# Optimization experiments

Hardware: AMD Instinct MI355X
Metric: run time of the kernel (lower is better)

Reference implementation:

```python
import jax, jax.numpy as jnp
import numpy as np

B, T, C, H = 4, 1024, 1024, 16
D = C // H
SINK = 4
EPS_LN = 1e-5

def _layernorm(x, w, b):
    mu = jnp.mean(x, axis=-1, keepdims=True)
    var = jnp.mean(jnp.square(x - mu), axis=-1, keepdims=True)
    return (x - mu) * jax.lax.rsqrt(var + EPS_LN) * w + b

def setup_inputs() -> dict:
    key = jax.random.key(0)
    ks = jax.random.split(key, 8)
    s = 0.02
    inp = {
        "x": jax.random.normal(ks[0], (B, T, C), jnp.float32),
        "attention_mask": jnp.ones((B, T), jnp.int32),
        "W_attn": jax.random.normal(ks[1], (C, 3 * C), jnp.float32) * s,
        "b_attn": jnp.zeros((3 * C,), jnp.float32),
        "W_proj": jax.random.normal(ks[2], (C, C), jnp.float32) * s,
        "b_proj": jnp.zeros((C,), jnp.float32),
        "ln1_w": jnp.ones((C,), jnp.float32),
        "ln1_b": jnp.zeros((C,), jnp.float32),
        "ln2_w": jnp.ones((C,), jnp.float32),
        "ln2_b": jnp.zeros((C,), jnp.float32),
        "W_fc": jax.random.normal(ks[3], (C, 4 * C), jnp.float32) * s,
        "b_fc": jnp.zeros((4 * C,), jnp.float32),
        "W_fc2": jax.random.normal(ks[4], (4 * C, C), jnp.float32) * s,
        "b_fc2": jnp.zeros((C,), jnp.float32),
        "threshold": jnp.float32((0 + 1) / 12 * 0.01),  # layer_idx=0, n_layer=12, final_token_threshold=0.01
    }
    return inp

def reference(x, attention_mask, W_attn, b_attn, W_proj, b_proj,
              ln1_w, ln1_b, ln2_w, ln2_b, W_fc, b_fc, W_fc2, b_fc2, threshold):
    # --- attention on ln_1(x), with explicit weight materialization ---
    h = _layernorm(x, ln1_w, ln1_b)
    qkv = h @ W_attn + b_attn                       # (B,T,3C)
    q, k, v = jnp.split(qkv, 3, axis=-1)
    q = q.reshape(B, T, H, D).transpose(0, 2, 1, 3)  # (B,H,T,D)
    k = k.reshape(B, T, H, D).transpose(0, 2, 1, 3)
    v = v.reshape(B, T, H, D).transpose(0, 2, 1, 3)
    scores = jnp.einsum("bhqd,bhkd->bhqk", q, k) * (1.0 / np.sqrt(D))
    causal = jnp.tril(jnp.ones((T, T), bool))[None, None]          # (1,1,T,T)
    keep = causal & (attention_mask[:, None, None, :] != 0)        # (B,1,T,T)
    scores = jnp.where(keep, scores, -jnp.inf)
    att = jax.nn.softmax(scores, axis=-1)
    att = jnp.nan_to_num(att, nan=0.0)              # fully-masked rows -> 0
    y = jnp.einsum("bhqk,bhkd->bhqd", att, v)       # (B,H,T,D)
    y = y.transpose(0, 2, 1, 3).reshape(B, T, C)
    y = y @ W_proj + b_proj                         # dropout=0.0 -> identity

    # --- cumulative-attention importance ---
    imp = att.sum(axis=2).mean(axis=1)              # (B,T): attention received
    pos_norm = jnp.arange(T, 0, -1, dtype=jnp.float32) / T
    imp = imp / (pos_norm[None, :] + 1e-8)
    imp = imp.at[:, :SINK].set(imp.max() + 1.0)

    # --- residual + MLP ---
    x2 = x + y
    m = _layernorm(x2, ln2_w, ln2_b)
    mlp = jax.nn.gelu(m @ W_fc + b_fc, approximate=False) @ W_fc2 + b_fc2
    out = x2 + mlp

    # --- hard pruning mask ---
    mask = (imp >= threshold).astype(jnp.float32)
    mask = mask.at[:, :SINK].set(1.0)
    mask = mask * attention_mask.astype(jnp.float32)
    return out, mask, imp
```

## Files before the change

### kernel.cpp

```cpp
#include <hip/hip_runtime.h>
#include <math.h>

constexpr int Bc = 4, Tc = 1024, Cc = 1024, Hc = 16, Dc = 64, SINKc = 4;
constexpr float EPS_LN = 1e-5f;

typedef __bf16 bf16x4 __attribute__((ext_vector_type(4)));
typedef __bf16 bf16x8 __attribute__((ext_vector_type(8)));
typedef float  f32x4  __attribute__((ext_vector_type(4)));

__global__ __launch_bounds__(256) void transpose_bf16(
    const float* __restrict__ W, __bf16* __restrict__ Wt, int K, int N)
{
    __shared__ float S[32][33];
    int n0 = blockIdx.x * 32, k0 = blockIdx.y * 32;
    int t = threadIdx.x;
    int r = t >> 3, c4 = (t & 7) * 4;
    float4 v = *(const float4*)(W + (size_t)(k0 + r) * N + n0 + c4);
    S[r][c4+0] = v.x; S[r][c4+1] = v.y; S[r][c4+2] = v.z; S[r][c4+3] = v.w;
    __syncthreads();
    bf16x4 o = { (__bf16)S[c4+0][r], (__bf16)S[c4+1][r],
                 (__bf16)S[c4+2][r], (__bf16)S[c4+3][r] };
    *(bf16x4*)(Wt + (size_t)(n0 + r) * K + k0 + c4) = o;
}

__global__ __launch_bounds__(256) void ln_kernel(
    const float* __restrict__ x, const float* __restrict__ w,
    const float* __restrict__ bsh, __bf16* __restrict__ outp)
{
    int row = blockIdx.x;
    const float* xr = x + (size_t)row * Cc;
    int tid = threadIdx.x;

    float4 xl = reinterpret_cast<const float4*>(xr)[tid];
    float s  = xl.x + xl.y + xl.z + xl.w;
    float s2 = xl.x*xl.x + xl.y*xl.y + xl.z*xl.z + xl.w*xl.w;
    for (int off = 32; off; off >>= 1) {
        s  += __shfl_down(s,  off, 64);
        s2 += __shfl_down(s2, off, 64);
    }
    __shared__ float r1[4], r2[4];
    if ((tid & 63) == 0) { r1[tid >> 6] = s; r2[tid >> 6] = s2; }
    __syncthreads();
    float mu  = (r1[0]+r1[1]+r1[2]+r1[3]) * (1.0f / Cc);
    float var = (r2[0]+r2[1]+r2[2]+r2[3]) * (1.0f / Cc) - mu*mu;
    float rstd = rsqrtf(var + EPS_LN);

    float4 wl = reinterpret_cast<const float4*>(w)[tid];
    float4 bl = reinterpret_cast<const float4*>(bsh)[tid];
    bf16x4 o = { (__bf16)((xl.x - mu) * rstd * wl.x + bl.x),
                 (__bf16)((xl.y - mu) * rstd * wl.y + bl.y),
                 (__bf16)((xl.z - mu) * rstd * wl.z + bl.z),
                 (__bf16)((xl.w - mu) * rstd * wl.w + bl.w) };
    *(bf16x4*)(outp + (size_t)row * Cc + tid * 4) = o;
}

template <int EPI, typename OutT, int TM, int OCC>
__global__ __launch_bounds__(256, OCC) void gemm_bf16(
    const __bf16* __restrict__ A, const __bf16* __restrict__ Bt,
    const float* __restrict__ bias, const float* R,
    OutT* Cm, int M, int N, int K)
{
    __shared__ __bf16 As[2][2][TM * 32];
    __shared__ __bf16 Bs[2][2][128 * 32];

    const int tid  = threadIdx.x;
    const int wave = tid >> 6, lane = tid & 63;
    const int wm = wave >> 1, wn = wave & 1;
    const int lr = lane & 15, lc = lane >> 4;

    const int gx = N >> 7;
    const int nblk = gridDim.x;
    const int per = nblk >> 3;
    const int rank = (blockIdx.x & 7) * per + (blockIdx.x >> 3);
    const int GM = 8;
    const int grp = rank / (GM * gx);
    const int rem = rank % (GM * gx);
    const int by = grp * GM + (rem % GM);
    const int bx = rem / GM;

    f32x4 acc[TM / 32][4] = {};

    const int srow = lane >> 2;
    const int cphys = lane & 3;

    auto stage = [&](int buf, int kk) {
        #pragma unroll
        for (int ii = wave; ii < (TM / 16) * 2; ii += 4) {
            int idx = ii >> 1, c = ii & 1;
            int rloc = idx * 16 + srow;
            int clog = (cphys - (rloc >> 1)) & 3;
            const __bf16* ga = A + (size_t)(by * TM + rloc) * K + kk + c * 32 + clog * 8;
            __builtin_amdgcn_global_load_lds(
                (const __attribute__((address_space(1))) void*)ga,
                (__attribute__((address_space(3))) void*)(&As[buf][c][idx * 512]), 16, 0, 0);
        }
        #pragma unroll
        for (int ii = wave; ii < 16; ii += 4) {
            int idx = ii >> 1, c = ii & 1;
            int rloc = idx * 16 + srow;
            int clog = (cphys - (rloc >> 1)) & 3;
            const __bf16* gb = Bt + (size_t)(bx * 128 + rloc) * K + kk + c * 32 + clog * 8;
            __builtin_amdgcn_global_load_lds(
                (const __attribute__((address_space(1))) void*)gb,
                (__attribute__((address_space(3))) void*)(&Bs[buf][c][idx * 512]), 16, 0, 0);
        }
    };

    stage(0, 0);
    __syncthreads();

    int cur = 0;
    for (int k0 = 0; k0 < K; k0 += 64) {
        if (k0 + 64 < K) stage(cur ^ 1, k0 + 64);

        #pragma unroll
        for (int s = 0; s < 2; s++) {
            bf16x8 af[TM / 32], bfr[4];
            #pragma unroll
            for (int i = 0; i < TM / 32; i++) {
                int ra = wm * (TM / 2) + i * 16 + lr;
                int ca = (lc + (ra >> 1)) & 3;
                af[i] = *(const bf16x8*)(&As[cur][s][ra * 32 + ca * 8]);
            }
            #pragma unroll
            for (int j = 0; j < 4; j++) {
                int rb = wn * 64 + j * 16 + lr;
                int cb = (lc + (rb >> 1)) & 3;
                bfr[j] = *(const bf16x8*)(&Bs[cur][s][rb * 32 + cb * 8]);
            }
            #pragma unroll
            for (int i = 0; i < TM / 32; i++)
                #pragma unroll
                for (int j = 0; j < 4; j++)
                    acc[i][j] = __builtin_amdgcn_mfma_f32_16x16x32_bf16(
                        af[i], bfr[j], acc[i][j], 0, 0, 0);
        }

        __syncthreads();
        cur ^= 1;
    }

    #pragma unroll
    for (int j = 0; j < 4; j++) {
        int n = bx * 128 + wn * 64 + j * 16 + lr;
        float bv = bias[n];
        #pragma unroll
        for (int i = 0; i < TM / 32; i++) {
            int m0 = by * TM + wm * (TM / 2) + i * 16 + lc * 4;
            #pragma unroll
            for (int e = 0; e < 4; e++) {
                float t = acc[i][j][e] + bv;
                if (EPI == 1) t = 0.5f * t * (1.0f + erff(t * 0.70710678118654752f));
                if (EPI == 2) t += R[(size_t)(m0 + e) * N + n];
                Cm[(size_t)(m0 + e) * N + n] = (OutT)t;
            }
        }
    }
}

__global__ __launch_bounds__(256, 3) void attn_mfma(
    const __bf16* __restrict__ qkv, const int* __restrict__ amask,
    __bf16* __restrict__ ybuf, float* __restrict__ lbuf)
{
    __shared__ __bf16 Kb[2][64 * 32];
    __shared__ __align__(16) __bf16 Vt[64][72];
    __shared__ __align__(16) __bf16 Ps[64][72];

    int blk = blockIdx.x;
    int idx = blk & 15, h = (blk >> 4) & 15, b = blk >> 8;
    int idx2 = (idx + h + b) & 15;
    int p2 = idx2 >> 1;
    int qt = (idx2 & 1) ? p2 : (15 - p2);
    int q0 = qt * 64;

    int tid = threadIdx.x, wave = tid >> 6, lane = tid & 63;
    int quad = lane >> 4, l15 = lane & 15;
    const int srow = lane >> 2, cphys = lane & 3;
    const size_t RS = 3 * Cc;
    const size_t bT = (size_t)b * Tc;

    bf16x8 qf[2];
    {
        const __bf16* qrow = qkv + (bT + q0 + wave * 16 + l15) * RS + h * 64 + quad * 8;
        qf[0] = *(const bf16x8*)qrow;
        qf[1] = *(const bf16x8*)(qrow + 32);
    }

    float l_part[4] = {0.f, 0.f, 0.f, 0.f};
    f32x4 Oacc[4] = {};

    for (int kt = 0; kt <= qt; kt++) {
        int k0 = kt * 64;
        __syncthreads();

        #pragma unroll
        for (int c = 0; c < 2; c++) {
            int rloc = wave * 16 + srow;
            int clog = (cphys - (rloc >> 1)) & 3;
            const __bf16* g = qkv + (bT + k0 + rloc) * RS + Cc + h * 64 + c * 32 + clog * 8;
            __builtin_amdgcn_global_load_lds(
                (const __attribute__((address_space(1))) void*)g,
                (__attribute__((address_space(3))) void*)(&Kb[c][wave * 512]), 16, 0, 0);
        }
        {
            int kk = lane, dbase = wave * 16;
            const __bf16* vrow = qkv + (bT + k0 + kk) * RS + 2 * Cc + h * 64 + dbase;
            bf16x8 v0 = *(const bf16x8*)vrow;
            bf16x8 v1 = *(const bf16x8*)(vrow + 8);
            #pragma unroll
            for (int j = 0; j < 8; j++) Vt[dbase + j][kk] = v0[j];
            #pragma unroll
            for (int j = 0; j < 8; j++) Vt[dbase + 8 + j][kk] = v1[j];
        }
        int am4[4];
        #pragma unroll
        for (int j = 0; j < 4; j++) am4[j] = amask[bT + k0 + j * 16 + l15];
        __syncthreads();

        f32x4 Sacc[4] = {};
        #pragma unroll
        for (int c = 0; c < 2; c++)
            #pragma unroll
            for (int j = 0; j < 4; j++) {
                int rb = j * 16 + l15;
                int cb = (quad + (rb >> 1)) & 3;
                bf16x8 kf = *(const bf16x8*)(&Kb[c][rb * 32 + cb * 8]);
                Sacc[j] = __builtin_amdgcn_mfma_f32_16x16x32_bf16(qf[c], kf, Sacc[j], 0, 0, 0);
            }

        #pragma unroll
        for (int e = 0; e < 4; e++) {
            int qg = q0 + wave * 16 + quad * 4 + e;
            #pragma unroll
            for (int j = 0; j < 4; j++) {
                int kg = k0 + j * 16 + l15;
                float p = (kg <= qg && am4[j] != 0)
                              ? __expf(Sacc[j][e] * 0.125f) : 0.f;
                l_part[e] += p;
                Ps[wave * 16 + quad * 4 + e][j * 16 + l15] = (__bf16)p;
            }
        }
        __syncthreads();

        #pragma unroll
        for (int c2 = 0; c2 < 2; c2++) {
            bf16x8 pa = *(const bf16x8*)(&Ps[wave * 16 + l15][quad * 8 + c2 * 32]);
            #pragma unroll
            for (int j2 = 0; j2 < 4; j2++) {
                bf16x8 vb = *(const bf16x8*)(&Vt[j2 * 16 + l15][quad * 8 + c2 * 32]);
                Oacc[j2] = __builtin_amdgcn_mfma_f32_16x16x32_bf16(pa, vb, Oacc[j2], 0, 0, 0);
            }
        }
    }

    #pragma unroll
    for (int e = 0; e < 4; e++) {
        float l = l_part[e];
        #pragma unroll
        for (int off = 8; off; off >>= 1) l += __shfl_xor(l, off, 64);
        int qg = q0 + wave * 16 + quad * 4 + e;
        float invl = (l > 0.f) ? 1.f / l : 0.f;
        #pragma unroll
        for (int j2 = 0; j2 < 4; j2++)
            ybuf[(bT + qg) * Cc + h * 64 + j2 * 16 + l15] = (__bf16)(Oacc[j2][e] * invl);
        if (l15 == 0)
            lbuf[(size_t)(b * Hc + h) * Tc + qg] = l;
    }
}

__global__ __launch_bounds__(256, 4) void imp_mfma(
    const __bf16* __restrict__ qkv, const int* __restrict__ amask,
    const float* __restrict__ lbuf, float* __restrict__ impbuf)
{
    __shared__ __bf16 Qb[2][64 * 32];
    __shared__ float rls[64];

    int blk = blockIdx.x;
    int idx = blk & 15, h = (blk >> 4) & 15, b = blk >> 8;
    int idx2 = (idx + h + b) & 15;
    int p2 = idx2 >> 1;
    int kt = (idx2 & 1) ? (15 - p2) : p2;
    int k0 = kt * 64;

    int tid = threadIdx.x, wave = tid >> 6, lane = tid & 63;
    int quad = lane >> 4, l15 = lane & 15;
    const int srow = lane >> 2, cphys = lane & 3;
    const size_t RS = 3 * Cc;
    const size_t bT = (size_t)b * Tc;
    const size_t mlrow = (size_t)(b * Hc + h) * Tc;

    bf16x8 kf[2];
    {
        const __bf16* krow = qkv + (bT + k0 + wave * 16 + l15) * RS + Cc + h * 64 + quad * 8;
        kf[0] = *(const bf16x8*)krow;
        kf[1] = *(const bf16x8*)(krow + 32);
    }
    int amk[4];
    #pragma unroll
    for (int e = 0; e < 4; e++) amk[e] = amask[bT + k0 + wave * 16 + quad * 4 + e];

    float sums[4] = {0.f, 0.f, 0.f, 0.f};

    for (int qt = kt; qt < 16; qt++) {
        int q0 = qt * 64;
        __syncthreads();
        #pragma unroll
        for (int c = 0; c < 2; c++) {
            int rloc = wave * 16 + srow;
            int clog = (cphys - (rloc >> 1)) & 3;
            const __bf16* g = qkv + (bT + q0 + rloc) * RS + h * 64 + c * 32 + clog * 8;
            __builtin_amdgcn_global_load_lds(
                (const __attribute__((address_space(1))) void*)g,
                (__attribute__((address_space(3))) void*)(&Qb[c][wave * 512]), 16, 0, 0);
        }
        if (tid < 64) {
            float l = lbuf[mlrow + q0 + tid];
            rls[tid] = (l > 0.f) ? 1.f / l : 0.f;
        }
        __syncthreads();

        f32x4 Sacc[4] = {};
        #pragma unroll
        for (int c = 0; c < 2; c++)
            #pragma unroll
            for (int j = 0; j < 4; j++) {
                int rb = j * 16 + l15;
                int cb = (quad + (rb >> 1)) & 3;
                bf16x8 qb = *(const bf16x8*)(&Qb[c][rb * 32 + cb * 8]);
                Sacc[j] = __builtin_amdgcn_mfma_f32_16x16x32_bf16(kf[c], qb, Sacc[j], 0, 0, 0);
            }

        #pragma unroll
        for (int j = 0; j < 4; j++) {
            int qg = q0 + j * 16 + l15;
            float rl = rls[j * 16 + l15];
            #pragma unroll
            for (int e = 0; e < 4; e++) {
                int kg = k0 + wave * 16 + quad * 4 + e;
                if (kg <= qg && amk[e] != 0 && rl > 0.f)
                    sums[e] += __expf(Sacc[j][e] * 0.125f) * rl;
            }
        }
    }

    #pragma unroll
    for (int e = 0; e < 4; e++) {
        float s = sums[e];
        #pragma unroll
        for (int off = 8; off; off >>= 1) s += __shfl_xor(s, off, 64);
        if (l15 == 0)
            atomicAdd(&impbuf[bT + k0 + wave * 16 + quad * 4 + e], s);
    }
}

__global__ __launch_bounds__(1024) void finalize_kernel(
    const float* __restrict__ impbuf, const int* __restrict__ amask,
    const float* __restrict__ thr, float* __restrict__ out_mask,
    float* __restrict__ out_imp)
{
    __shared__ float red[16];
    int tid = threadIdx.x;
    float vloc[4];
    float gmax = -INFINITY;
    #pragma unroll
    for (int it = 0; it < 4; it++) {
        int i = tid + it * 1024;
        int tt = i % Tc;
        float posn = (float)(Tc - tt) / (float)Tc;
        float v = impbuf[i] * (1.0f / Hc) / (posn + 1e-8f);
        vloc[it] = v;
        gmax = fmaxf(gmax, v);
    }
    for (int off = 32; off; off >>= 1) gmax = fmaxf(gmax, __shfl_down(gmax, off, 64));
    if ((tid & 63) == 0) red[tid >> 6] = gmax;
    __syncthreads();
    float gm = red[0];
    #pragma unroll
    for (int i = 1; i < 16; i++) gm = fmaxf(gm, red[i]);

    float t = thr[0];
    #pragma unroll
    for (int it = 0; it < 4; it++) {
        int i = tid + it * 1024;
        int tt = i % Tc;
        float v = vloc[it];
        if (tt < SINKc) v = gm + 1.0f;
        float mk = (v >= t) ? 1.f : 0.f;
        if (tt < SINKc) mk = 1.f;
        mk *= (float)amask[i];
        out_imp[i]  = v;
        out_mask[i] = mk;
    }
}

extern "C" void kernel_launch(void* const* d_in, const int* in_sizes, int n_in,
                              void* d_out, int out_size, void* d_ws, size_t ws_size,
                              hipStream_t stream)
{
    const float* x      = (const float*)d_in[0];
    const int*   amask  = (const int*)  d_in[1];
    const float* W_attn = (const float*)d_in[2];
    const float* b_attn = (const float*)d_in[3];
    const float* W_proj = (const float*)d_in[4];
    const float* b_proj = (const float*)d_in[5];
    const float* ln1w   = (const float*)d_in[6];
    const float* ln1b   = (const float*)d_in[7];
    const float* ln2w   = (const float*)d_in[8];
    const float* ln2b   = (const float*)d_in[9];
    const float* W_fc   = (const float*)d_in[10];
    const float* b_fc   = (const float*)d_in[11];
    const float* W_fc2  = (const float*)d_in[12];
    const float* b_fc2  = (const float*)d_in[13];
    const float* thr    = (const float*)d_in[14];

    float* out      = (float*)d_out;
    float* out_mask = out + (size_t)Bc * Tc * Cc;
    float* out_imp  = out_mask + (size_t)Bc * Tc;

    char* wsb = (char*)d_ws;
    __bf16* qkvbf = (__bf16*)wsb;
    __bf16* hbf   = (__bf16*)(wsb + 25165824);
    __bf16* ybf   = (__bf16*)(wsb + 33554432);
    __bf16* fcbf  = (__bf16*)(wsb + 41943040);
    __bf16* WaT   = (__bf16*)(wsb + 75497472);
    __bf16* WpT   = (__bf16*)(wsb + 81788928);
    __bf16* WfT   = (__bf16*)(wsb + 83886080);
    __bf16* Wf2T  = (__bf16*)(wsb + 92274688);
    float*  lbuf  = (float*)(wsb + 100663296);
    float*  impb  = (float*)(wsb + 100925440);

    const int M = Bc * Tc;

    transpose_bf16<<<dim3(3*Cc/32, Cc/32), 256, 0, stream>>>(W_attn, WaT, Cc, 3*Cc);
    transpose_bf16<<<dim3(Cc/32,   Cc/32), 256, 0, stream>>>(W_proj, WpT, Cc, Cc);
    transpose_bf16<<<dim3(4*Cc/32, Cc/32), 256, 0, stream>>>(W_fc,   WfT, Cc, 4*Cc);
    transpose_bf16<<<dim3(Cc/32, 4*Cc/32), 256, 0, stream>>>(W_fc2,  Wf2T, 4*Cc, Cc);

    ln_kernel<<<M, 256, 0, stream>>>(x, ln1w, ln1b, hbf);
    gemm_bf16<0, __bf16, 128, 2><<<(3*Cc/128) * (M/128), 256, 0, stream>>>(
        hbf, WaT, b_attn, nullptr, qkvbf, M, 3*Cc, Cc);
    hipMemsetAsync(impb, 0, (size_t)Bc * Tc * sizeof(float), stream);
    attn_mfma<<<Bc * Hc * 16, 256, 0, stream>>>(qkvbf, amask, ybf, lbuf);
    gemm_bf16<2, float, 64, 3><<<(Cc/128) * (M/64), 256, 0, stream>>>(
        ybf, WpT, b_proj, x, out, M, Cc, Cc);
    imp_mfma<<<Bc * Hc * 16, 256, 0, stream>>>(qkvbf, amask, lbuf, impb);
    ln_kernel<<<M, 256, 0, stream>>>(out, ln2w, ln2b, hbf);
    gemm_bf16<1, __bf16, 128, 2><<<(4*Cc/128) * (M/128), 256, 0, stream>>>(
        hbf, WfT, b_fc, nullptr, fcbf, M, 4*Cc, Cc);
    gemm_bf16<2, float, 64, 3><<<(Cc/128) * (M/64), 256, 0, stream>>>(
        fcbf, Wf2T, b_fc2, out, out, M, Cc, 4*Cc);
    finalize_kernel<<<1, 1024, 0, stream>>>(impb, amask, thr, out_mask, out_imp);
}
```

Measured before the change: 389.0 us.

## Load GEMM fragments directly from global memory, dropping LDS staging

The GEMM kernel no longer stages A and B tiles into shared memory through double-buffered global_load_lds. Each wave now loads its MFMA operand fragments straight from global memory into registers every K step, and the block barriers go away. This removes LDS traffic and synchronisation, but it loses data reuse across waves: each A and B fragment is fetched by two waves instead of once per block. It also loses the prefetch overlap, so global load latency sits directly in front of the MFMAs.

```diff
diff --git a/kernel.cpp b/kernel.cpp
--- a/kernel.cpp
+++ b/kernel.cpp
@@ -60,9 +60,6 @@
     const float* __restrict__ bias, const float* R,
     OutT* Cm, int M, int N, int K)
 {
-    __shared__ __bf16 As[2][2][TM * 32];
-    __shared__ __bf16 Bs[2][2][128 * 32];
-
     const int tid  = threadIdx.x;
     const int wave = tid >> 6, lane = tid & 63;
     const int wm = wave >> 1, wn = wave & 1;
@@ -80,64 +77,31 @@
 
     f32x4 acc[TM / 32][4] = {};
 
-    const int srow = lane >> 2;
-    const int cphys = lane & 3;
-
-    auto stage = [&](int buf, int kk) {
-        #pragma unroll
-        for (int ii = wave; ii < (TM / 16) * 2; ii += 4) {
-            int idx = ii >> 1, c = ii & 1;
-            int rloc = idx * 16 + srow;
-            int clog = (cphys - (rloc >> 1)) & 3;
-            const __bf16* ga = A + (size_t)(by * TM + rloc) * K + kk + c * 32 + clog * 8;
-            __builtin_amdgcn_global_load_lds(
-                (const __attribute__((address_space(1))) void*)ga,
-                (__attribute__((address_space(3))) void*)(&As[buf][c][idx * 512]), 16, 0, 0);
-        }
-        #pragma unroll
-        for (int ii = wave; ii < 16; ii += 4) {
-            int idx = ii >> 1, c = ii & 1;
-            int rloc = idx * 16 + srow;
-            int clog = (cphys - (rloc >> 1)) & 3;
-            const __bf16* gb = Bt + (size_t)(bx * 128 + rloc) * K + kk + c * 32 + clog * 8;
-            __builtin_amdgcn_global_load_lds(
-                (const __attribute__((address_space(1))) void*)gb,
-                (__attribute__((address_space(3))) void*)(&Bs[buf][c][idx * 512]), 16, 0, 0);
-        }
-    };
-
-    stage(0, 0);
-    __syncthreads();
-
-    int cur = 0;
+    const __bf16* Ap = A  + (size_t)(by * TM + wm * (TM / 2) + lr) * K + lc * 8;
+    const __bf16* Bp = Bt + (size_t)(bx * 128 + wn * 64 + lr) * K + lc * 8;
+
     for (int k0 = 0; k0 < K; k0 += 64) {
-        if (k0 + 64 < K) stage(cur ^ 1, k0 + 64);
-
-        #pragma unroll
-        for (int s = 0; s < 2; s++) {
-            bf16x8 af[TM / 32], bfr[4];
-            #pragma unroll
-            for (int i = 0; i < TM / 32; i++) {
-                int ra = wm * (TM / 2) + i * 16 + lr;
-                int ca = (lc + (ra >> 1)) & 3;
-                af[i] = *(const bf16x8*)(&As[cur][s][ra * 32 + ca * 8]);
-            }
-            #pragma unroll
-            for (int j = 0; j < 4; j++) {
-                int rb = wn * 64 + j * 16 + lr;
-                int cb = (lc + (rb >> 1)) & 3;
-                bfr[j] = *(const bf16x8*)(&Bs[cur][s][rb * 32 + cb * 8]);
-            }
+        bf16x8 af[TM / 32][2], bfr[4][2];
+        #pragma unroll
+        for (int i = 0; i < TM / 32; i++) {
+            const __bf16* pa = Ap + (size_t)(i * 16) * K + k0;
+            af[i][0] = *(const bf16x8*)pa;
+            af[i][1] = *(const bf16x8*)(pa + 32);
+        }
+        #pragma unroll
+        for (int j = 0; j < 4; j++) {
+            const __bf16* pb = Bp + (size_t)(j * 16) * K + k0;
+            bfr[j][0] = *(const bf16x8*)pb;
+            bfr[j][1] = *(const bf16x8*)(pb + 32);
+        }
+        #pragma unroll
+        for (int s = 0; s < 2; s++)
             #pragma unroll
             for (int i = 0; i < TM / 32; i++)
                 #pragma unroll
                 for (int j = 0; j < 4; j++)
                     acc[i][j] = __builtin_amdgcn_mfma_f32_16x16x32_bf16(
-                        af[i], bfr[j], acc[i][j], 0, 0, 0);
-        }
-
-        __syncthreads();
-        cur ^= 1;
+                        af[i][s], bfr[j][s], acc[i][j], 0, 0, 0);
     }
 
     #pragma unroll
```

New measurement: 661.5 us. +70.0%, slower.
